# Kernel optimization log

Hardware: AMD Instinct MI355X
Metric: run time of the kernel (lower is better)

Reference implementation:

```python
import jax, jax.numpy as jnp
import numpy as np

B, N, CS, CZ, CH, H, PQ, PV = 1, 768, 384, 128, 16, 12, 4, 8
INF, EPS = 1e5, 1e-8


def quat_to_rot(q):
    q = q / jnp.linalg.norm(q, axis=-1, keepdims=True)
    w, x, y, z = q[..., 0], q[..., 1], q[..., 2], q[..., 3]
    r0 = jnp.stack([1 - 2 * (y * y + z * z), 2 * (x * y - w * z), 2 * (x * z + w * y)], -1)
    r1 = jnp.stack([2 * (x * y + w * z), 1 - 2 * (x * x + z * z), 2 * (y * z - w * x)], -1)
    r2 = jnp.stack([2 * (x * z - w * y), 2 * (y * z + w * x), 1 - 2 * (x * x + y * y)], -1)
    return jnp.stack([r0, r1, r2], -2)


def setup_inputs() -> dict:
    key = jax.random.key(0)
    ks = jax.random.split(key, 12)
    nrm = lambda k, shp, sc=1.0: jax.random.normal(k, shp, jnp.float32) * sc
    s = nrm(ks[0], (B, N, CS))
    z = nrm(ks[1], (B, N, N, CZ))
    rot = quat_to_rot(nrm(ks[2], (B, N, 4)))
    trans = nrm(ks[3], (B, N, 3))
    mask = jnp.ones((B, N), jnp.float32)
    dout = H * (CZ + CH + PV * 4)
    return dict(
        s=s, z=z, rot=rot, trans=trans, mask=mask,
        w_q=nrm(ks[4], (H * CH, CS), 0.02), b_q=jnp.zeros((H * CH,), jnp.float32),
        w_kv=nrm(ks[5], (2 * H * CH, CS), 0.02), b_kv=jnp.zeros((2 * H * CH,), jnp.float32),
        w_qp=nrm(ks[6], (H * PQ * 3, CS), 0.02), b_qp=jnp.zeros((H * PQ * 3,), jnp.float32),
        w_kvp=nrm(ks[7], (H * (PQ + PV) * 3, CS), 0.02), b_kvp=jnp.zeros((H * (PQ + PV) * 3,), jnp.float32),
        w_b=nrm(ks[8], (H, CZ), 0.02), b_b=jnp.zeros((H,), jnp.float32),
        head_weights=jnp.full((H,), 0.541324854612918, jnp.float32),
        w_out=nrm(ks[9], (CS, dout), 0.02), b_out=jnp.zeros((CS,), jnp.float32),
    )


def ipa_forward(s, z, rot, trans, mask, w_q, b_q, w_kv, b_kv, w_qp, b_qp,
                w_kvp, b_kvp, w_b, b_b, head_weights, w_out, b_out):
    # scalar q/k/v: [B,N,H,CH]
    q = (s @ w_q.T + b_q).reshape(B, N, H, CH)
    kv = (s @ w_kv.T + b_kv).reshape(B, N, H, 2 * CH)
    k, v = kv[..., :CH], kv[..., CH:]
    # point projections in local frame, then rigid apply: x_glob = R x + t
    qp = (s @ w_qp.T + b_qp).reshape(B, N, H, PQ, 3)
    kvp = (s @ w_kvp.T + b_kvp).reshape(B, N, H, PQ + PV, 3)
    t = trans[:, :, None, None, :]
    q_pts = jnp.einsum('bnij,bnhpj->bnhpi', rot, qp) + t
    kv_pts = jnp.einsum('bnij,bnhpj->bnhpi', rot, kvp) + t
    k_pts, v_pts = kv_pts[..., :PQ, :], kv_pts[..., PQ:, :]
    # pair bias: [B,H,N,N]
    b = jnp.moveaxis(z @ w_b.T + b_b, -1, 1)
    # scalar attention logits
    a = jnp.einsum('bihc,bjhc->bhij', q, k) * np.sqrt(1.0 / (3 * CH))
    a = a + np.sqrt(1.0 / 3) * b
    # point-distance attention: [B,N,N,H]
    diff = q_pts[:, :, None] - k_pts[:, None]  # [B,N,N,H,PQ,3]
    d2 = jnp.sum(diff * diff, axis=-1)  # [B,N,N,H,PQ]
    hw = jax.nn.softplus(head_weights) * np.sqrt(1.0 / (3 * (PQ * 9.0 / 2)))
    pt_att = -0.5 * jnp.sum(d2 * hw[None, None, None, :, None], axis=-1)
    a = a + jnp.moveaxis(pt_att, -1, 1)
    # mask
    sq_mask = INF * (mask[:, :, None] * mask[:, None, :] - 1.0)  # [B,N,N]
    a = jax.nn.softmax(a + sq_mask[:, None], axis=-1)  # [B,H,N,N]
    # outputs
    o = jnp.einsum('bhij,bjhc->bihc', a, v).reshape(B, N, H * CH)
    o_pt = jnp.einsum('bhij,bjhpx->bihpx', a, v_pts)  # global frame
    o_pt_loc = jnp.einsum('bnji,bnhpj->bnhpi', rot, o_pt - t)  # R^T (x - t)
    o_pt_norm = jnp.sqrt(jnp.sum(o_pt_loc * o_pt_loc, axis=-1) + EPS)  # [B,N,H,PV]
    o_pair = jnp.einsum('bhij,bijc->bihc', a, z).reshape(B, N, H * CZ)
    cat = jnp.concatenate([o, o_pt_loc.reshape(B, N, H * PV * 3),
                           o_pt_norm.reshape(B, N, H * PV), o_pair], axis=-1)
    return cat @ w_out.T + b_out  # [B,N,CS]


def reference(s, z, rot, trans, mask, w_q, b_q, w_kv, b_kv, w_qp, b_qp,
              w_kvp, b_kvp, w_b, b_b, head_weights, w_out, b_out):
    return ipa_forward(s, z, rot, trans, mask, w_q, b_q, w_kv, b_kv, w_qp, b_qp,
                       w_kvp, b_kvp, w_b, b_b, head_weights, w_out, b_out)
```

## Files before the change

### kernel.cpp

```cpp
#include <hip/hip_runtime.h>
#include <math.h>

#define Nn 768
#define NN 589824
#define DOUT 2112

#define WS_Q   0
#define WS_K   147456
#define WS_QP  442368
#define WS_KP  552960
#define WS_A   2506752
#define WS_VT  6045696
#define WS_CH  6230016
#define WS_CL  7041024
#define WS_WH  7852032
#define WS_WL  8257536

typedef unsigned short u16;
typedef unsigned int u32;

using bf16x8 = __attribute__((ext_vector_type(8))) short;
using f32x4  = __attribute__((ext_vector_type(4))) float;

__device__ __forceinline__ float bf2f(u16 u) {
  union { float f; u32 i; } x; x.i = ((u32)u) << 16; return x.f;
}
__device__ __forceinline__ u16 f2bf(float f) {
  union { float f; u32 i; } x; x.f = f;
  u32 r = x.i + 0x7FFFu + ((x.i >> 16) & 1u);
  return (u16)(r >> 16);
}
__device__ __forceinline__ void wr_hl(u16* ch, u16* cl, int idx, float v) {
  u16 hb = f2bf(v);
  ch[idx] = hb;
  cl[idx] = f2bf(v - bf2f(hb));
}

__global__ __launch_bounds__(256) void k_proj(
    const float* __restrict__ s, const float* __restrict__ rot, const float* __restrict__ trans,
    const float* __restrict__ w_q, const float* __restrict__ b_q,
    const float* __restrict__ w_kv, const float* __restrict__ b_kv,
    const float* __restrict__ w_qp, const float* __restrict__ b_qp,
    const float* __restrict__ w_kvp, const float* __restrict__ b_kvp,
    float* __restrict__ ws)
{
  __shared__ float s16[16][384];
  __shared__ float praw[16][192];
  __shared__ float rot16[16][9];
  __shared__ float t16[16][3];
  const int t = threadIdx.x;
  const int ib = blockIdx.x, fg = blockIdx.y;
  const int i0 = ib * 16;
  u16* VT = (u16*)(ws + WS_VT);

  {
    const float4* sp = (const float4*)(s + (size_t)i0 * 384);
    float4* dp = (float4*)&s16[0][0];
    for (int idx = t; idx < 1536; idx += 256) dp[idx] = sp[idx];
  }
  if (fg >= 3) {
    if (t < 144) rot16[t / 9][t % 9] = rot[i0 * 9 + t];
    else if (t < 192) { int g = t - 144; t16[g / 3][g % 3] = trans[i0 * 3 + g]; }
  }
  __syncthreads();

  const int rg = t >> 6;
  const int fl = t & 63;
  for (int p = 0; p < 3; p++) {
    const int f_loc = p * 64 + fl;
    const int F = fg * 192 + f_loc;
    const float* wrow; float bias;
    if (F < 192)      { wrow = w_q   + (size_t)F * 384;          bias = b_q[F]; }
    else if (F < 576) { int g = F - 192; wrow = w_kv  + (size_t)g * 384; bias = b_kv[g]; }
    else if (F < 720) { int g = F - 576; wrow = w_qp  + (size_t)g * 384; bias = b_qp[g]; }
    else              { int g = F - 720; wrow = w_kvp + (size_t)g * 384; bias = b_kvp[g]; }
    float a0 = bias, a1 = bias, a2 = bias, a3 = bias;
    const float4* w4 = (const float4*)wrow;
    #pragma unroll 4
    for (int c4 = 0; c4 < 96; c4++) {
      float4 wv = w4[c4];
      const float4 v0 = *(const float4*)&s16[rg * 4 + 0][c4 * 4];
      const float4 v1 = *(const float4*)&s16[rg * 4 + 1][c4 * 4];
      const float4 v2 = *(const float4*)&s16[rg * 4 + 2][c4 * 4];
      const float4 v3 = *(const float4*)&s16[rg * 4 + 3][c4 * 4];
      a0 += wv.x * v0.x + wv.y * v0.y + wv.z * v0.z + wv.w * v0.w;
      a1 += wv.x * v1.x + wv.y * v1.y + wv.z * v1.z + wv.w * v1.w;
      a2 += wv.x * v2.x + wv.y * v2.y + wv.z * v2.z + wv.w * v2.w;
      a3 += wv.x * v3.x + wv.y * v3.y + wv.z * v3.z + wv.w * v3.w;
    }
    float av[4] = {a0, a1, a2, a3};
    if (F < 576) {
      if (F < 192) {
        float* base = ws + WS_Q + ((F >> 4) * Nn) * 16 + (F & 15);
        #pragma unroll
        for (int r = 0; r < 4; r++) base[(i0 + rg * 4 + r) * 16] = av[r];
      } else {
        int g = F - 192, hh = g >> 5, x = g & 31;
        if (x < 16) {
          float* base = ws + WS_K + (hh * Nn) * 16 + x;
          #pragma unroll
          for (int r = 0; r < 4; r++) base[(i0 + rg * 4 + r) * 16] = av[r];
        } else {
          u16* vt = VT + (size_t)(hh * 40 + (x - 16)) * 768;
          #pragma unroll
          for (int r = 0; r < 4; r++) vt[i0 + rg * 4 + r] = f2bf(av[r]);
        }
      }
    } else {
      #pragma unroll
      for (int r = 0; r < 4; r++) praw[rg * 4 + r][f_loc] = av[r];
    }
  }
  if (fg >= 3) {
    __syncthreads();
    #pragma unroll
    for (int k = 0; k < 4; k++) {
      int tk = t + k * 256;
      int row = tk >> 6, tri = tk & 63;
      int g3 = tri * 3;
      int i = i0 + row;
      float vx = praw[row][g3], vy = praw[row][g3 + 1], vz = praw[row][g3 + 2];
      const float* R = rot16[row];
      const float* T = t16[row];
      float o0 = R[0] * vx + R[1] * vy + R[2] * vz + T[0];
      float o1 = R[3] * vx + R[4] * vy + R[5] * vz + T[1];
      float o2 = R[6] * vx + R[7] * vy + R[8] * vz + T[2];
      int pt_g = (fg - 3) * 192 + g3;
      if (pt_g < 144) {
        int hh = pt_g / 12, pp = (pt_g / 3) & 3;
        float* dst = ws + WS_QP + (hh * Nn + i) * 12 + pp * 3;
        dst[0] = o0; dst[1] = o1; dst[2] = o2;
      } else {
        int gg = pt_g - 144; int hh = gg / 36, pp = (gg / 3) % 12;
        if (pp < 4) {
          float* dst = ws + WS_KP + (hh * Nn + i) * 12 + pp * 3;
          dst[0] = o0; dst[1] = o1; dst[2] = o2;
        } else {
          u16* vt = VT + (size_t)(hh * 40 + 16 + (pp - 4) * 3) * 768 + i;
          vt[0] = f2bf(o0); vt[768] = f2bf(o1); vt[1536] = f2bf(o2);
        }
      }
    }
  }
}

__global__ __launch_bounds__(256) void k_bias(
    const float* __restrict__ z, const float* __restrict__ w_b, const float* __restrict__ b_b,
    u16* __restrict__ A)
{
  const int t = threadIdx.x;
  const size_t pair = (size_t)blockIdx.x * 256 + t;
  const float4* zp = (const float4*)(z + pair * 128);
  const float4* wb4 = (const float4*)w_b;
  float acc[12];
  #pragma unroll
  for (int h = 0; h < 12; h++) acc[h] = b_b[h];
  #pragma unroll 4
  for (int c4 = 0; c4 < 32; c4++) {
    float4 zv = zp[c4];
    #pragma unroll
    for (int h = 0; h < 12; h++) {
      const float4 wv = wb4[h * 32 + c4];
      acc[h] += zv.x * wv.x + zv.y * wv.y + zv.z * wv.z + zv.w * wv.w;
    }
  }
  #pragma unroll
  for (int h = 0; h < 12; h++) A[(size_t)h * NN + pair] = f2bf(acc[h]);
}

__global__ __launch_bounds__(256) void k_attn(
    const float* __restrict__ ws, u16* __restrict__ A,
    const float* __restrict__ mask, const float* __restrict__ head_weights)
{
  const int h = blockIdx.x;
  const int i0 = blockIdx.y * 4;
  const int t = threadIdx.x;
  const int lane = t & 63, wv = t >> 6;
  __shared__ float qrow[4][16];
  __shared__ float qp4[4][12];
  __shared__ float mi4[4];
  __shared__ float red[4][4];
  __shared__ float Msh[4], Ssh[4];

  if (t < 64) { int r = t >> 4, c = t & 15; qrow[r][c] = ws[WS_Q + (h * Nn + i0 + r) * 16 + c]; }
  else if (t < 112) { int g = t - 64; int r = g / 12, d = g - r * 12; qp4[r][d] = ws[WS_QP + (h * Nn + i0 + r) * 12 + d]; }
  else if (t < 116) mi4[t - 112] = mask[i0 + t - 112];
  const float hw = log1pf(__expf(head_weights[h]));
  const float cpt = -0.5f * hw * 0.13608276348795434f;
  __syncthreads();

  float L[4][3];
  float lmax[4] = {-1e30f, -1e30f, -1e30f, -1e30f};
  #pragma unroll
  for (int jj = 0; jj < 3; jj++) {
    const int j = t + jj * 256;
    const float4* kp = (const float4*)(ws + WS_K + (size_t)(h * Nn + j) * 16);
    float kr[16];
    #pragma unroll
    for (int u = 0; u < 4; u++) { float4 vv = kp[u]; kr[u*4] = vv.x; kr[u*4+1] = vv.y; kr[u*4+2] = vv.z; kr[u*4+3] = vv.w; }
    const float4* pp4 = (const float4*)(ws + WS_KP + (size_t)(h * Nn + j) * 12);
    float kpt[12];
    #pragma unroll
    for (int u = 0; u < 3; u++) { float4 vv = pp4[u]; kpt[u*4] = vv.x; kpt[u*4+1] = vv.y; kpt[u*4+2] = vv.z; kpt[u*4+3] = vv.w; }
    const float mj = mask[j];
    #pragma unroll
    for (int r = 0; r < 4; r++) {
      float qk = 0.f;
      #pragma unroll
      for (int c = 0; c < 16; c++) qk += qrow[r][c] * kr[c];
      float d2 = 0.f;
      #pragma unroll
      for (int d = 0; d < 12; d++) { float df = qp4[r][d] - kpt[d]; d2 += df * df; }
      float bias = bf2f(A[h * NN + (i0 + r) * Nn + j]);
      float Lv = qk * 0.14433756729740643f + 0.57735026918962584f * bias + cpt * d2
               + 100000.0f * (mi4[r] * mj - 1.0f);
      L[r][jj] = Lv;
      lmax[r] = fmaxf(lmax[r], Lv);
    }
  }
  #pragma unroll
  for (int r = 0; r < 4; r++) {
    float v = lmax[r];
    #pragma unroll
    for (int o = 32; o > 0; o >>= 1) v = fmaxf(v, __shfl_xor(v, o));
    if (lane == 0) red[wv][r] = v;
  }
  __syncthreads();
  if (t < 4) Msh[t] = fmaxf(fmaxf(red[0][t], red[1][t]), fmaxf(red[2][t], red[3][t]));
  __syncthreads();
  float lsum[4] = {0.f, 0.f, 0.f, 0.f};
  #pragma unroll
  for (int jj = 0; jj < 3; jj++) {
    #pragma unroll
    for (int r = 0; r < 4; r++) {
      float e = __expf(L[r][jj] - Msh[r]);
      L[r][jj] = e; lsum[r] += e;
    }
  }
  #pragma unroll
  for (int r = 0; r < 4; r++) {
    float v = lsum[r];
    #pragma unroll
    for (int o = 32; o > 0; o >>= 1) v += __shfl_xor(v, o);
    if (lane == 0) red[wv][r] = v;
  }
  __syncthreads();
  if (t < 4) Ssh[t] = red[0][t] + red[1][t] + red[2][t] + red[3][t];
  __syncthreads();
  float inv[4];
  #pragma unroll
  for (int r = 0; r < 4; r++) inv[r] = 1.0f / Ssh[r];
  #pragma unroll
  for (int jj = 0; jj < 3; jj++) {
    int j = t + jj * 256;
    #pragma unroll
    for (int r = 0; r < 4; r++)
      A[h * NN + (i0 + r) * Nn + j] = f2bf(L[r][jj] * inv[r]);
  }
}

__global__ __launch_bounds__(192) void k_out_ov(
    const u16* __restrict__ A, const u16* __restrict__ VT,
    const float* __restrict__ rot, const float* __restrict__ trans,
    float* __restrict__ ws)
{
  const int ib = blockIdx.x, h = blockIdx.y;
  const int i0 = ib * 16;
  const int t = threadIdx.x;
  const int w = t >> 6, lane = t & 63;
  const int n = lane & 15, quad = lane >> 4;
  __shared__ float opt[16][26];
  u16* CH = (u16*)(ws + WS_CH);
  u16* CL = (u16*)(ws + WS_CL);

  const int col40 = w * 16 + n;
  const bool bvalid = col40 < 40;
  const u16* abase = A + (size_t)h * NN + (size_t)(i0 + n) * Nn + quad * 8;
  const u16* bbase = VT + (size_t)(h * 40 + (bvalid ? col40 : 0)) * 768 + quad * 8;

  f32x4 acc = {0.f, 0.f, 0.f, 0.f};
  #pragma unroll 4
  for (int kk = 0; kk < 24; kk++) {
    bf16x8 af = *(const bf16x8*)(abase + kk * 32);
    bf16x8 bf = *(const bf16x8*)(bbase + kk * 32);
    if (!bvalid) bf = bf16x8{0, 0, 0, 0, 0, 0, 0, 0};
    acc = __builtin_amdgcn_mfma_f32_16x16x32_bf16(af, bf, acc, 0, 0, 0);
  }

  const int mrow = quad * 4;
  if (w == 0) {
    u16* chb = CH + (size_t)i0 * DOUT + h * 16 + n;
    u16* clb = CL + (size_t)i0 * DOUT + h * 16 + n;
    #pragma unroll
    for (int r = 0; r < 4; r++) wr_hl(chb, clb, (mrow + r) * DOUT, acc[r]);
  } else if (w == 1 || n < 8) {
    const int col = (w - 1) * 16 + n;
    #pragma unroll
    for (int r = 0; r < 4; r++) opt[mrow + r][col] = acc[r];
  }
  __syncthreads();
  if (t < 128) {
    const int ii = t >> 3, p = t & 7;
    const int i = i0 + ii;
    float R[9], T[3];
    #pragma unroll
    for (int u = 0; u < 9; u++) R[u] = rot[i * 9 + u];
    #pragma unroll
    for (int u = 0; u < 3; u++) T[u] = trans[i * 3 + u];
    float g0 = opt[ii][p * 3 + 0] - T[0];
    float g1 = opt[ii][p * 3 + 1] - T[1];
    float g2 = opt[ii][p * 3 + 2] - T[2];
    float lx = R[0] * g0 + R[3] * g1 + R[6] * g2;
    float ly = R[1] * g0 + R[4] * g1 + R[7] * g2;
    float lz = R[2] * g0 + R[5] * g1 + R[8] * g2;
    u16* chb = CH + (size_t)i * DOUT;
    u16* clb = CL + (size_t)i * DOUT;
    wr_hl(chb, clb, 192 + (h * 8 + p) * 3 + 0, lx);
    wr_hl(chb, clb, 192 + (h * 8 + p) * 3 + 1, ly);
    wr_hl(chb, clb, 192 + (h * 8 + p) * 3 + 2, lz);
    wr_hl(chb, clb, 480 + h * 8 + p, sqrtf(lx * lx + ly * ly + lz * lz + 1e-8f));
  }
}

__global__ __launch_bounds__(256) void k_out_pair(
    const float* __restrict__ z, const u16* __restrict__ A, float* __restrict__ ws)
{
  const int i = blockIdx.x;
  const int t = threadIdx.x;
  const int w = t >> 6, lane = t & 63;
  const int x = lane & 15, quad = lane >> 4;
  u16* CH = (u16*)(ws + WS_CH);
  u16* CL = (u16*)(ws + WS_CL);

  const u16* ap = A + (size_t)x * NN + (size_t)i * Nn + quad * 8;
  const float* zrow = z + (size_t)i * Nn * 128;
  const int c0a = (w * 2) * 16 + x;
  const int c0b = (w * 2 + 1) * 16 + x;

  f32x4 accA = {0.f, 0.f, 0.f, 0.f};
  f32x4 accB = {0.f, 0.f, 0.f, 0.f};
  #pragma unroll 2
  for (int ks = 0; ks < 24; ks++) {
    bf16x8 af = *(const bf16x8*)(ap + ks * 32);
    const float* zb = zrow + (size_t)(ks * 32 + quad * 8) * 128;
    float va[8], vb[8];
    #pragma unroll
    for (int j = 0; j < 8; j++) {
      va[j] = zb[j * 128 + c0a];
      vb[j] = zb[j * 128 + c0b];
    }
    bf16x8 zah, zal, zbh, zbl;
    #pragma unroll
    for (int j = 0; j < 8; j++) {
      u16 h0 = f2bf(va[j]);
      zah[j] = (short)h0; zal[j] = (short)f2bf(va[j] - bf2f(h0));
      u16 h1 = f2bf(vb[j]);
      zbh[j] = (short)h1; zbl[j] = (short)f2bf(vb[j] - bf2f(h1));
    }
    accA = __builtin_amdgcn_mfma_f32_16x16x32_bf16(af, zah, accA, 0, 0, 0);
    accA = __builtin_amdgcn_mfma_f32_16x16x32_bf16(af, zal, accA, 0, 0, 0);
    accB = __builtin_amdgcn_mfma_f32_16x16x32_bf16(af, zbh, accB, 0, 0, 0);
    accB = __builtin_amdgcn_mfma_f32_16x16x32_bf16(af, zbl, accB, 0, 0, 0);
  }

  if (quad < 3) {
    u16* chb = CH + (size_t)i * DOUT + 576;
    u16* clb = CL + (size_t)i * DOUT + 576;
    #pragma unroll
    for (int r = 0; r < 4; r++) {
      const int head = quad * 4 + r;
      wr_hl(chb, clb, head * 128 + c0a, accA[r]);
      wr_hl(chb, clb, head * 128 + c0b, accB[r]);
    }
  }
}

__global__ __launch_bounds__(256) void k_wcvt(const float* __restrict__ w_out, float* __restrict__ ws)
{
  const int idx = blockIdx.x * 256 + threadIdx.x;
  float4 v = ((const float4*)w_out)[idx];
  u16 h0 = f2bf(v.x), h1 = f2bf(v.y), h2 = f2bf(v.z), h3 = f2bf(v.w);
  ushort4 hv; hv.x = h0; hv.y = h1; hv.z = h2; hv.w = h3;
  ushort4 lv;
  lv.x = f2bf(v.x - bf2f(h0));
  lv.y = f2bf(v.y - bf2f(h1));
  lv.z = f2bf(v.z - bf2f(h2));
  lv.w = f2bf(v.w - bf2f(h3));
  ((ushort4*)(ws + WS_WH))[idx] = hv;
  ((ushort4*)(ws + WS_WL))[idx] = lv;
}

__global__ __launch_bounds__(256) void k_final_mfma(
    const float* __restrict__ ws, const float* __restrict__ b_out, float* __restrict__ outp)
{
  const int i0 = blockIdx.x * 16, c0 = blockIdx.y * 16;
  const int t = threadIdx.x;
  const int w = t >> 6, lane = t & 63;
  const int n = lane & 15, quad = lane >> 4;
  const u16* CH  = (const u16*)(ws + WS_CH);
  const u16* CL  = (const u16*)(ws + WS_CL);
  const u16* WHp = (const u16*)(ws + WS_WH);
  const u16* WLp = (const u16*)(ws + WS_WL);
  const u16* ah_p = CH  + (size_t)(i0 + n) * DOUT + quad * 8;
  const u16* al_p = CL  + (size_t)(i0 + n) * DOUT + quad * 8;
  const u16* bh_p = WHp + (size_t)(c0 + n) * DOUT + quad * 8;
  const u16* bl_p = WLp + (size_t)(c0 + n) * DOUT + quad * 8;

  const int s0 = (w * 66) >> 2, s1 = ((w + 1) * 66) >> 2;
  f32x4 acc = {0.f, 0.f, 0.f, 0.f};
  for (int ss = s0; ss < s1; ss++) {
    bf16x8 ah = *(const bf16x8*)(ah_p + ss * 32);
    bf16x8 al = *(const bf16x8*)(al_p + ss * 32);
    bf16x8 bh = *(const bf16x8*)(bh_p + ss * 32);
    bf16x8 bl = *(const bf16x8*)(bl_p + ss * 32);
    acc = __builtin_amdgcn_mfma_f32_16x16x32_bf16(ah, bh, acc, 0, 0, 0);
    acc = __builtin_amdgcn_mfma_f32_16x16x32_bf16(ah, bl, acc, 0, 0, 0);
    acc = __builtin_amdgcn_mfma_f32_16x16x32_bf16(al, bh, acc, 0, 0, 0);
  }

  __shared__ float red[4][64][4];
  #pragma unroll
  for (int r = 0; r < 4; r++) red[w][lane][r] = acc[r];
  __syncthreads();
  if (w == 0) {
    const float bo = b_out[c0 + n];
    #pragma unroll
    for (int r = 0; r < 4; r++) {
      float v = red[0][lane][r] + red[1][lane][r] + red[2][lane][r] + red[3][lane][r] + bo;
      outp[(size_t)(i0 + quad * 4 + r) * 384 + c0 + n] = v;
    }
  }
}

extern "C" void kernel_launch(void* const* d_in, const int* in_sizes, int n_in,
                              void* d_out, int out_size, void* d_ws, size_t ws_size,
                              hipStream_t stream)
{
  const float* s      = (const float*)d_in[0];
  const float* z      = (const float*)d_in[1];
  const float* rot    = (const float*)d_in[2];
  const float* trans  = (const float*)d_in[3];
  const float* mask   = (const float*)d_in[4];
  const float* w_q    = (const float*)d_in[5];
  const float* b_q    = (const float*)d_in[6];
  const float* w_kv   = (const float*)d_in[7];
  const float* b_kv   = (const float*)d_in[8];
  const float* w_qp   = (const float*)d_in[9];
  const float* b_qp   = (const float*)d_in[10];
  const float* w_kvp  = (const float*)d_in[11];
  const float* b_kvp  = (const float*)d_in[12];
  const float* w_b    = (const float*)d_in[13];
  const float* b_b    = (const float*)d_in[14];
  const float* hwts   = (const float*)d_in[15];
  const float* w_out  = (const float*)d_in[16];
  const float* b_out  = (const float*)d_in[17];
  float* ws = (float*)d_ws;
  u16* A = (u16*)(ws + WS_A);
  u16* VT = (u16*)(ws + WS_VT);
  float* outp = (float*)d_out;

  k_wcvt<<<dim3(792), dim3(256), 0, stream>>>(w_out, ws);
  k_proj<<<dim3(48, 6), dim3(256), 0, stream>>>(s, rot, trans, w_q, b_q, w_kv, b_kv,
                                                w_qp, b_qp, w_kvp, b_kvp, ws);
  k_bias<<<dim3(2304), dim3(256), 0, stream>>>(z, w_b, b_b, A);
  k_attn<<<dim3(12, 192), dim3(256), 0, stream>>>(ws, A, mask, hwts);
  k_out_ov<<<dim3(48, 12), dim3(192), 0, stream>>>(A, VT, rot, trans, ws);
  k_out_pair<<<dim3(768), dim3(256), 0, stream>>>(z, A, ws);
  k_final_mfma<<<dim3(48, 24), dim3(256), 0, stream>>>(ws, b_out, outp);
}
```

Measured before the change: 668.5 us.

## Fuse pair-bias and logits into one kernel, defer softmax normalization

Merges the pair-bias projection and the attention-logit kernel into one per-row kernel that computes the bias from z on the fly. It writes unnormalized exp(logit) straight to A, dropping the max subtraction, and stores per-row inverse sums. The sums are applied later in the output kernels. This removes one full read and write of the bf16 attention matrix and a launch, at the cost of fewer blocks (768), reloading q per head from global memory, and overflow risk without the max shift.

```diff
diff --git a/kernel.cpp b/kernel.cpp
--- a/kernel.cpp
+++ b/kernel.cpp
@@ -15,6 +15,7 @@
 #define WS_CL  7041024
 #define WS_WH  7852032
 #define WS_WL  8257536
+#define WS_LS  8663040
 
 typedef unsigned short u16;
 typedef unsigned int u32;
@@ -144,125 +145,101 @@
   }
 }
 
-__global__ __launch_bounds__(256) void k_bias(
-    const float* __restrict__ z, const float* __restrict__ w_b, const float* __restrict__ b_b,
-    u16* __restrict__ A)
-{
+__global__ __launch_bounds__(256) void k_zfused(
+    const float* __restrict__ z, const float* __restrict__ ws,
+    const float* __restrict__ w_b, const float* __restrict__ b_b,
+    const float* __restrict__ mask, const float* __restrict__ head_weights,
+    u16* __restrict__ A, float* __restrict__ LS)
+{
+  const int i = blockIdx.x;
   const int t = threadIdx.x;
-  const size_t pair = (size_t)blockIdx.x * 256 + t;
-  const float4* zp = (const float4*)(z + pair * 128);
-  const float4* wb4 = (const float4*)w_b;
-  float acc[12];
+  const int lane = t & 63, w = t >> 6;
+  const float s1 = 0.14433756729740643f;
+  const float s2 = 0.57735026918962584f;
+
+  __shared__ float red[4][12];
+  __shared__ float cpt_sh[12], c0_sh[12];
+  if (t < 12) {
+    float hw = log1pf(__expf(head_weights[t]));
+    cpt_sh[t] = -0.5f * hw * 0.13608276348795434f;
+    c0_sh[t] = s2 * b_b[t];
+  }
+  const float mi = mask[i];
+  __syncthreads();
+
+  float lsum[12];
   #pragma unroll
-  for (int h = 0; h < 12; h++) acc[h] = b_b[h];
-  #pragma unroll 4
-  for (int c4 = 0; c4 < 32; c4++) {
-    float4 zv = zp[c4];
-    #pragma unroll
-    for (int h = 0; h < 12; h++) {
-      const float4 wv = wb4[h * 32 + c4];
-      acc[h] += zv.x * wv.x + zv.y * wv.y + zv.z * wv.z + zv.w * wv.w;
-    }
-  }
-  #pragma unroll
-  for (int h = 0; h < 12; h++) A[(size_t)h * NN + pair] = f2bf(acc[h]);
-}
-
-__global__ __launch_bounds__(256) void k_attn(
-    const float* __restrict__ ws, u16* __restrict__ A,
-    const float* __restrict__ mask, const float* __restrict__ head_weights)
-{
-  const int h = blockIdx.x;
-  const int i0 = blockIdx.y * 4;
-  const int t = threadIdx.x;
-  const int lane = t & 63, wv = t >> 6;
-  __shared__ float qrow[4][16];
-  __shared__ float qp4[4][12];
-  __shared__ float mi4[4];
-  __shared__ float red[4][4];
-  __shared__ float Msh[4], Ssh[4];
-
-  if (t < 64) { int r = t >> 4, c = t & 15; qrow[r][c] = ws[WS_Q + (h * Nn + i0 + r) * 16 + c]; }
-  else if (t < 112) { int g = t - 64; int r = g / 12, d = g - r * 12; qp4[r][d] = ws[WS_QP + (h * Nn + i0 + r) * 12 + d]; }
-  else if (t < 116) mi4[t - 112] = mask[i0 + t - 112];
-  const float hw = log1pf(__expf(head_weights[h]));
-  const float cpt = -0.5f * hw * 0.13608276348795434f;
-  __syncthreads();
-
-  float L[4][3];
-  float lmax[4] = {-1e30f, -1e30f, -1e30f, -1e30f};
-  #pragma unroll
+  for (int h = 0; h < 12; h++) lsum[h] = 0.f;
+
   for (int jj = 0; jj < 3; jj++) {
     const int j = t + jj * 256;
-    const float4* kp = (const float4*)(ws + WS_K + (size_t)(h * Nn + j) * 16);
-    float kr[16];
-    #pragma unroll
-    for (int u = 0; u < 4; u++) { float4 vv = kp[u]; kr[u*4] = vv.x; kr[u*4+1] = vv.y; kr[u*4+2] = vv.z; kr[u*4+3] = vv.w; }
-    const float4* pp4 = (const float4*)(ws + WS_KP + (size_t)(h * Nn + j) * 12);
-    float kpt[12];
-    #pragma unroll
-    for (int u = 0; u < 3; u++) { float4 vv = pp4[u]; kpt[u*4] = vv.x; kpt[u*4+1] = vv.y; kpt[u*4+2] = vv.z; kpt[u*4+3] = vv.w; }
-    const float mj = mask[j];
-    #pragma unroll
-    for (int r = 0; r < 4; r++) {
+    const float mterm = 100000.0f * (mi * mask[j] - 1.0f);
+    float bias[12];
+    #pragma unroll
+    for (int h = 0; h < 12; h++) bias[h] = 0.f;
+    const float4* zp = (const float4*)(z + ((size_t)i * Nn + j) * 128);
+    const float4* wb4 = (const float4*)w_b;
+    #pragma unroll 2
+    for (int c4 = 0; c4 < 32; c4++) {
+      float4 zv = zp[c4];
+      #pragma unroll
+      for (int h = 0; h < 12; h++) {
+        float4 wv = wb4[h * 32 + c4];
+        bias[h] += zv.x * wv.x + zv.y * wv.y + zv.z * wv.z + zv.w * wv.w;
+      }
+    }
+    #pragma unroll 2
+    for (int h = 0; h < 12; h++) {
+      const float4* kp4 = (const float4*)(ws + WS_K + (size_t)(h * Nn + j) * 16);
+      float kr[16];
+      #pragma unroll
+      for (int u = 0; u < 4; u++) {
+        float4 vv = kp4[u];
+        kr[u*4] = vv.x; kr[u*4+1] = vv.y; kr[u*4+2] = vv.z; kr[u*4+3] = vv.w;
+      }
+      const float4* pp4 = (const float4*)(ws + WS_KP + (size_t)(h * Nn + j) * 12);
+      float kpt[12];
+      #pragma unroll
+      for (int u = 0; u < 3; u++) {
+        float4 vv = pp4[u];
+        kpt[u*4] = vv.x; kpt[u*4+1] = vv.y; kpt[u*4+2] = vv.z; kpt[u*4+3] = vv.w;
+      }
+      const float* qr = ws + WS_Q + (size_t)(h * Nn + i) * 16;
+      const float* qp = ws + WS_QP + (size_t)(h * Nn + i) * 12;
       float qk = 0.f;
       #pragma unroll
-      for (int c = 0; c < 16; c++) qk += qrow[r][c] * kr[c];
+      for (int c = 0; c < 16; c++) qk += qr[c] * kr[c];
       float d2 = 0.f;
       #pragma unroll
-      for (int d = 0; d < 12; d++) { float df = qp4[r][d] - kpt[d]; d2 += df * df; }
-      float bias = bf2f(A[h * NN + (i0 + r) * Nn + j]);
-      float Lv = qk * 0.14433756729740643f + 0.57735026918962584f * bias + cpt * d2
-               + 100000.0f * (mi4[r] * mj - 1.0f);
-      L[r][jj] = Lv;
-      lmax[r] = fmaxf(lmax[r], Lv);
+      for (int d = 0; d < 12; d++) { float df = qp[d] - kpt[d]; d2 += df * df; }
+      float Lv = qk * s1 + s2 * bias[h] + c0_sh[h] + cpt_sh[h] * d2 + mterm;
+      float p = __expf(Lv);
+      lsum[h] += p;
+      A[(size_t)h * NN + (size_t)i * Nn + j] = f2bf(p);
     }
   }
   #pragma unroll
-  for (int r = 0; r < 4; r++) {
-    float v = lmax[r];
-    #pragma unroll
-    for (int o = 32; o > 0; o >>= 1) v = fmaxf(v, __shfl_xor(v, o));
-    if (lane == 0) red[wv][r] = v;
+  for (int h = 0; h < 12; h++) {
+    float v = lsum[h];
+    #pragma unroll
+    for (int o = 32; o > 0; o >>= 1) v += __shfl_xor(v, o);
+    lsum[h] = v;
+  }
+  if (lane == 0) {
+    #pragma unroll
+    for (int h = 0; h < 12; h++) red[w][h] = lsum[h];
   }
   __syncthreads();
-  if (t < 4) Msh[t] = fmaxf(fmaxf(red[0][t], red[1][t]), fmaxf(red[2][t], red[3][t]));
-  __syncthreads();
-  float lsum[4] = {0.f, 0.f, 0.f, 0.f};
-  #pragma unroll
-  for (int jj = 0; jj < 3; jj++) {
-    #pragma unroll
-    for (int r = 0; r < 4; r++) {
-      float e = __expf(L[r][jj] - Msh[r]);
-      L[r][jj] = e; lsum[r] += e;
-    }
-  }
-  #pragma unroll
-  for (int r = 0; r < 4; r++) {
-    float v = lsum[r];
-    #pragma unroll
-    for (int o = 32; o > 0; o >>= 1) v += __shfl_xor(v, o);
-    if (lane == 0) red[wv][r] = v;
-  }
-  __syncthreads();
-  if (t < 4) Ssh[t] = red[0][t] + red[1][t] + red[2][t] + red[3][t];
-  __syncthreads();
-  float inv[4];
-  #pragma unroll
-  for (int r = 0; r < 4; r++) inv[r] = 1.0f / Ssh[r];
-  #pragma unroll
-  for (int jj = 0; jj < 3; jj++) {
-    int j = t + jj * 256;
-    #pragma unroll
-    for (int r = 0; r < 4; r++)
-      A[h * NN + (i0 + r) * Nn + j] = f2bf(L[r][jj] * inv[r]);
+  if (t < 12) {
+    float l = red[0][t] + red[1][t] + red[2][t] + red[3][t];
+    LS[(size_t)t * 768 + i] = 1.0f / l;
   }
 }
 
 __global__ __launch_bounds__(192) void k_out_ov(
     const u16* __restrict__ A, const u16* __restrict__ VT,
     const float* __restrict__ rot, const float* __restrict__ trans,
-    float* __restrict__ ws)
+    const float* __restrict__ LS, float* __restrict__ ws)
 {
   const int ib = blockIdx.x, h = blockIdx.y;
   const int i0 = ib * 16;
@@ -270,6 +247,7 @@
   const int w = t >> 6, lane = t & 63;
   const int n = lane & 15, quad = lane >> 4;
   __shared__ float opt[16][26];
+  __shared__ float invl_sh[16];
   u16* CH = (u16*)(ws + WS_CH);
   u16* CL = (u16*)(ws + WS_CL);
 
@@ -287,29 +265,32 @@
     acc = __builtin_amdgcn_mfma_f32_16x16x32_bf16(af, bf, acc, 0, 0, 0);
   }
 
+  if (t < 16) invl_sh[t] = LS[(size_t)h * 768 + i0 + t];
   const int mrow = quad * 4;
+  if (w >= 1 && (w == 1 || n < 8)) {
+    const int col = (w - 1) * 16 + n;
+    #pragma unroll
+    for (int r = 0; r < 4; r++) opt[mrow + r][col] = acc[r];
+  }
+  __syncthreads();
   if (w == 0) {
     u16* chb = CH + (size_t)i0 * DOUT + h * 16 + n;
     u16* clb = CL + (size_t)i0 * DOUT + h * 16 + n;
     #pragma unroll
-    for (int r = 0; r < 4; r++) wr_hl(chb, clb, (mrow + r) * DOUT, acc[r]);
-  } else if (w == 1 || n < 8) {
-    const int col = (w - 1) * 16 + n;
-    #pragma unroll
-    for (int r = 0; r < 4; r++) opt[mrow + r][col] = acc[r];
-  }
-  __syncthreads();
+    for (int r = 0; r < 4; r++) wr_hl(chb, clb, (mrow + r) * DOUT, acc[r] * invl_sh[mrow + r]);
+  }
   if (t < 128) {
     const int ii = t >> 3, p = t & 7;
     const int i = i0 + ii;
+    const float il = invl_sh[ii];
     float R[9], T[3];
     #pragma unroll
     for (int u = 0; u < 9; u++) R[u] = rot[i * 9 + u];
     #pragma unroll
     for (int u = 0; u < 3; u++) T[u] = trans[i * 3 + u];
-    float g0 = opt[ii][p * 3 + 0] - T[0];
-    float g1 = opt[ii][p * 3 + 1] - T[1];
-    float g2 = opt[ii][p * 3 + 2] - T[2];
+    float g0 = opt[ii][p * 3 + 0] * il - T[0];
+    float g1 = opt[ii][p * 3 + 1] * il - T[1];
+    float g2 = opt[ii][p * 3 + 2] * il - T[2];
     float lx = R[0] * g0 + R[3] * g1 + R[6] * g2;
     float ly = R[1] * g0 + R[4] * g1 + R[7] * g2;
     float lz = R[2] * g0 + R[5] * g1 + R[8] * g2;
@@ -323,7 +304,8 @@
 }
 
 __global__ __launch_bounds__(256) void k_out_pair(
-    const float* __restrict__ z, const u16* __restrict__ A, float* __restrict__ ws)
+    const float* __restrict__ z, const u16* __restrict__ A,
+    const float* __restrict__ LS, float* __restrict__ ws)
 {
   const int i = blockIdx.x;
   const int t = threadIdx.x;
@@ -366,11 +348,14 @@
   if (quad < 3) {
     u16* chb = CH + (size_t)i * DOUT + 576;
     u16* clb = CL + (size_t)i * DOUT + 576;
+    float il[4];
+    #pragma unroll
+    for (int r = 0; r < 4; r++) il[r] = LS[(size_t)(quad * 4 + r) * 768 + i];
     #pragma unroll
     for (int r = 0; r < 4; r++) {
       const int head = quad * 4 + r;
-      wr_hl(chb, clb, head * 128 + c0a, accA[r]);
-      wr_hl(chb, clb, head * 128 + c0b, accB[r]);
+      wr_hl(chb, clb, head * 128 + c0a, accA[r] * il[r]);
+      wr_hl(chb, clb, head * 128 + c0b, accB[r] * il[r]);
     }
   }
 }
@@ -457,14 +442,14 @@
   float* ws = (float*)d_ws;
   u16* A = (u16*)(ws + WS_A);
   u16* VT = (u16*)(ws + WS_VT);
+  float* LS = ws + WS_LS;
   float* outp = (float*)d_out;
 
   k_wcvt<<<dim3(792), dim3(256), 0, stream>>>(w_out, ws);
   k_proj<<<dim3(48, 6), dim3(256), 0, stream>>>(s, rot, trans, w_q, b_q, w_kv, b_kv,
                                                 w_qp, b_qp, w_kvp, b_kvp, ws);
-  k_bias<<<dim3(2304), dim3(256), 0, stream>>>(z, w_b, b_b, A);
-  k_attn<<<dim3(12, 192), dim3(256), 0, stream>>>(ws, A, mask, hwts);
-  k_out_ov<<<dim3(48, 12), dim3(192), 0, stream>>>(A, VT, rot, trans, ws);
-  k_out_pair<<<dim3(768), dim3(256), 0, stream>>>(z, A, ws);
+  k_zfused<<<dim3(768), dim3(256), 0, stream>>>(z, ws, w_b, b_b, mask, hwts, A, LS);
+  k_out_ov<<<dim3(48, 12), dim3(192), 0, stream>>>(A, VT, rot, trans, LS, ws);
+  k_out_pair<<<dim3(768), dim3(256), 0, stream>>>(z, A, LS, ws);
   k_final_mfma<<<dim3(48, 24), dim3(256), 0, stream>>>(ws, b_out, outp);
 }
```

Result: no change. 658.4 us (-1.5%).
